# Kernel optimization log

Hardware: AMD Instinct MI355X
Metric: run time of the kernel (lower is better)

## Reference

```python
import jax, jax.numpy as jnp
import numpy as np
import math

B, N, EMB, DK = 4, 4096, 512, 64

def setup_inputs() -> dict:
    key = jax.random.key(0)
    ks = jax.random.split(key, 4)
    E = jax.random.normal(ks[0], (B, N, EMB), dtype=jnp.float32)
    mask = jnp.tril(jnp.ones((1, N, N), dtype=jnp.int32))  # causal mask, 0 = masked
    s = 1.0 / math.sqrt(EMB)
    wq_kernel = jax.random.normal(ks[1], (EMB, DK), dtype=jnp.float32) * s
    wk_kernel = jax.random.normal(ks[2], (EMB, DK), dtype=jnp.float32) * s
    wv_kernel = jax.random.normal(ks[3], (EMB, EMB), dtype=jnp.float32) * s
    return {
        "E": E, "mask": mask,
        "wq_kernel": wq_kernel, "wq_bias": jnp.zeros((DK,), jnp.float32),
        "wk_kernel": wk_kernel, "wk_bias": jnp.zeros((DK,), jnp.float32),
        "wv_kernel": wv_kernel, "wv_bias": jnp.zeros((EMB,), jnp.float32),
    }

def reference(E, mask, wq_kernel, wq_bias, wk_kernel, wk_bias, wv_kernel, wv_bias):
    # Dense projections (flax Dense: x @ kernel + bias)
    Q = jnp.einsum('bne,ed->bnd', E, wq_kernel) + wq_bias   # [B,N,DK]
    K = jnp.einsum('bne,ed->bnd', E, wk_kernel) + wk_bias   # [B,N,DK]
    V = jnp.einsum('bne,ed->bnd', E, wv_kernel) + wv_bias   # [B,N,EMB]
    scores = jnp.einsum('bqd,bkd->bqk', Q, K) / math.sqrt(Q.shape[-1])  # [B,N,N]
    scores = jnp.where(mask == 0, float('-inf'), scores)
    attention = jax.nn.softmax(scores, axis=-1)
    return jnp.einsum('bqk,bke->bqe', attention, V)  # [B,N,EMB]
```

## Files before the change

### kernel.cpp

```cpp
#include <hip/hip_runtime.h>
#include <hip/hip_bf16.h>

typedef float f32x4 __attribute__((ext_vector_type(4)));
typedef __bf16 bf16x8 __attribute__((ext_vector_type(8)));
typedef __bf16 bf16x4 __attribute__((ext_vector_type(4)));
typedef unsigned short ushort4v __attribute__((ext_vector_type(4)));
typedef unsigned short ushort8v __attribute__((ext_vector_type(8)));

#define MFMA16(a, b, c) __builtin_amdgcn_mfma_f32_16x16x32_bf16((a), (b), (c), 0, 0, 0)

__device__ __forceinline__ unsigned short f2bf(float f) {
    union { float f; unsigned int u; } v; v.f = f;
    unsigned int r = (v.u + 0x7fffu + ((v.u >> 16) & 1u)) >> 16;
    return (unsigned short)r;
}
__device__ __forceinline__ int imin(int a, int b) { return a < b ? a : b; }
__device__ __forceinline__ float fexp2(float x) {
    float r; asm("v_exp_f32 %0, %1" : "=v"(r) : "v"(x)); return r;
}

__device__ __forceinline__ void ldsbar() {
    asm volatile("s_waitcnt lgkmcnt(0)" ::: "memory");
    __builtin_amdgcn_s_barrier();
}

__global__ __launch_bounds__(256) void prep_w(const float* __restrict__ wq,
                                              const float* __restrict__ wk,
                                              const float* __restrict__ wv,
                                              unsigned short* __restrict__ Fqk,
                                              unsigned short* __restrict__ Fv)
{
    const int t = blockIdx.x * 256 + threadIdx.x;
    if (t < 8192) {
        const int lane = t & 63, kt = (t >> 6) & 15, ct = t >> 10;
        const int g = lane >> 4, li = lane & 15;
        const int c = ct * 16 + li;
        const int k0 = kt * 32 + g * 8;
        ushort8v u;
        if (c < 64) {
#pragma unroll
            for (int j = 0; j < 8; ++j) u[j] = f2bf(wq[(size_t)(k0 + j) * 64 + c]);
        } else {
#pragma unroll
            for (int j = 0; j < 8; ++j) u[j] = f2bf(wk[(size_t)(k0 + j) * 64 + (c - 64)]);
        }
        *(ushort8v*)&Fqk[(size_t)t * 8] = u;
    } else {
        const int t2 = t - 8192;
        const int lane = t2 & 63, kt = (t2 >> 6) & 15, ct = t2 >> 10;
        const int g = lane >> 4, li = lane & 15;
        const int c = ct * 16 + li;
        const int k0 = kt * 32 + g * 8;
        ushort8v u;
#pragma unroll
        for (int j = 0; j < 8; ++j) u[j] = f2bf(wv[(size_t)(k0 + j) * 512 + c]);
        *(ushort8v*)&Fv[(size_t)t2 * 8] = u;
    }
}

__global__ __launch_bounds__(512) void proj_kernel(const float* __restrict__ E,
        const unsigned short* __restrict__ Fqk, const unsigned short* __restrict__ Fv,
        const float* __restrict__ bq, const float* __restrict__ bk, const float* __restrict__ bv,
        unsigned short* __restrict__ Qb, unsigned short* __restrict__ Kb,
        unsigned short* __restrict__ Vt)
{
    __shared__ __align__(16) unsigned short Al[2][128][40];

    const int tid = threadIdx.x;
    const int w = tid >> 6, l = tid & 63, g = l >> 4, li = l & 15;
    const int wm = w >> 2, wn = w & 3;
    const int bx = blockIdx.x, by = blockIdx.y;
    const int row0 = bx * 128;
    const int arow = tid >> 2, ak = (tid & 3) * 8;
    const float* ebase = &E[(size_t)(row0 + arow) * 512 + ak];
    const float QSCALE = 0.125f * 1.4426950408889634f;

#define LOAD_E(kt, dst)                                                          \
    {                                                                            \
        const float* ep = ebase + (kt) * 32;                                     \
        f32x4 v0 = *(const f32x4*)ep;                                            \
        f32x4 v1 = *(const f32x4*)(ep + 4);                                      \
        _Pragma("unroll")                                                        \
        for (int j = 0; j < 4; ++j) { dst[j] = f2bf(v0[j]); dst[4 + j] = f2bf(v1[j]); } \
    }

    if (by == 0) {
        f32x4 acc[4][2];
#pragma unroll
        for (int mb = 0; mb < 4; ++mb)
#pragma unroll
            for (int nb = 0; nb < 2; ++nb) acc[mb][nb] = (f32x4)0.0f;

        bf16x8 bw[2], bwn[2];
        {
            ushort8v e0; LOAD_E(0, e0);
            *(ushort8v*)&Al[0][arow][ak] = e0;
#pragma unroll
            for (int nb = 0; nb < 2; ++nb) {
                const int ct = wn * 2 + nb;
                bw[nb] = *(const bf16x8*)&Fqk[((size_t)(ct * 16 + 0) * 64 + l) * 8];
            }
        }
        ldsbar();

        for (int kt = 0; kt < 16; ++kt) {
            const int buf = kt & 1;
            ushort8v en;
            if (kt < 15) LOAD_E(kt + 1, en);
            const int ktn = imin(kt + 1, 15);
#pragma unroll
            for (int nb = 0; nb < 2; ++nb) {
                const int ct = wn * 2 + nb;
                bwn[nb] = *(const bf16x8*)&Fqk[((size_t)(ct * 16 + ktn) * 64 + l) * 8];
            }
            bf16x8 af[4];
#pragma unroll
            for (int mb = 0; mb < 4; ++mb)
                af[mb] = *(const bf16x8*)&Al[buf][wm * 64 + mb * 16 + li][8 * g];
#pragma unroll
            for (int mb = 0; mb < 4; ++mb)
#pragma unroll
                for (int nb = 0; nb < 2; ++nb) acc[mb][nb] = MFMA16(af[mb], bw[nb], acc[mb][nb]);
            if (kt < 15) *(ushort8v*)&Al[buf ^ 1][arow][ak] = en;
            ldsbar();
            bw[0] = bwn[0]; bw[1] = bwn[1];
        }

#pragma unroll
        for (int mb = 0; mb < 4; ++mb) {
#pragma unroll
            for (int nb = 0; nb < 2; ++nb) {
                const int coll = wn * 32 + nb * 16 + li;
                const int grow0 = row0 + wm * 64 + mb * 16 + 4 * g;
                if (coll < 64) {
                    const float bb = bq[coll];
#pragma unroll
                    for (int r = 0; r < 4; ++r)
                        Qb[(size_t)(grow0 + r) * 64 + coll] = f2bf((acc[mb][nb][r] + bb) * QSCALE);
                } else {
                    const float bb = bk[coll - 64];
#pragma unroll
                    for (int r = 0; r < 4; ++r)
                        Kb[(size_t)(grow0 + r) * 64 + (coll - 64)] = f2bf(acc[mb][nb][r] + bb);
                }
            }
        }
    } else {
        const int vy = by - 1;
        f32x4 acc[4][4];
#pragma unroll
        for (int mb = 0; mb < 4; ++mb)
#pragma unroll
            for (int nb = 0; nb < 4; ++nb) acc[mb][nb] = (f32x4)0.0f;

        bf16x8 bw[4], bwn[4];
        {
            ushort8v e0; LOAD_E(0, e0);
            *(ushort8v*)&Al[0][arow][ak] = e0;
#pragma unroll
            for (int nb = 0; nb < 4; ++nb) {
                const int ct = vy * 16 + wn * 4 + nb;
                bw[nb] = *(const bf16x8*)&Fv[((size_t)(ct * 16 + 0) * 64 + l) * 8];
            }
        }
        ldsbar();

        for (int kt = 0; kt < 16; ++kt) {
            const int buf = kt & 1;
            ushort8v en;
            if (kt < 15) LOAD_E(kt + 1, en);
            const int ktn = imin(kt + 1, 15);
#pragma unroll
            for (int nb = 0; nb < 4; ++nb) {
                const int ct = vy * 16 + wn * 4 + nb;
                bwn[nb] = *(const bf16x8*)&Fv[((size_t)(ct * 16 + ktn) * 64 + l) * 8];
            }
            bf16x8 af[4];
#pragma unroll
            for (int mb = 0; mb < 4; ++mb)
                af[mb] = *(const bf16x8*)&Al[buf][wm * 64 + mb * 16 + li][8 * g];
#pragma unroll
            for (int mb = 0; mb < 4; ++mb)
#pragma unroll
                for (int nb = 0; nb < 4; ++nb) acc[mb][nb] = MFMA16(af[mb], bw[nb], acc[mb][nb]);
            if (kt < 15) *(ushort8v*)&Al[buf ^ 1][arow][ak] = en;
            ldsbar();
#pragma unroll
            for (int nb = 0; nb < 4; ++nb) bw[nb] = bwn[nb];
        }

#pragma unroll
        for (int mb = 0; mb < 4; ++mb) {
#pragma unroll
            for (int nb = 0; nb < 4; ++nb) {
                const int col = vy * 256 + wn * 64 + nb * 16 + li;
                const int grow0 = row0 + wm * 64 + mb * 16 + 4 * g;
                const float bb = bv[col];
                ushort4v u;
#pragma unroll
                for (int r = 0; r < 4; ++r) u[r] = f2bf(acc[mb][nb][r] + bb);
                const int bbatch = grow0 >> 12, n = grow0 & 4095;
                *(ushort4v*)(Vt + ((size_t)bbatch * 512 + col) * 4096 + n) = u;
            }
        }
    }
#undef LOAD_E
}

__global__ __launch_bounds__(256) void attn_kernel(const unsigned short* __restrict__ Qb,
                                                   const unsigned short* __restrict__ Kb,
                                                   const unsigned short* __restrict__ Vt,
                                                   float* __restrict__ out)
{
    __shared__ __align__(16) unsigned short Kl[2][64][64];
    __shared__ __align__(16) unsigned short Pl[2][64][76];
    __shared__ float scl[2][64];
    __shared__ __align__(16) float dfl[2][4];
    __shared__ float lsum_l[64];

    const int tid = threadIdx.x;
    const int w = tid >> 6, lane = tid & 63, g = lane >> 4, li = lane & 15;
    const int bid = blockIdx.x;
    const int x = bid >> 4, b = (bid >> 2) & 3, ch = bid & 3;
    const int k4 = x >> 4, r4 = x & 15;
    const int qt = (k4 == 0) ? r4 : (k4 == 1) ? (63 - r4) : (k4 == 2) ? (16 + r4) : (47 - r4);
    const int q0 = qt * 64;
    const int niter = qt + 1;
    const int qrow = 16 * w + li;

    const unsigned short* qptr = Qb + ((size_t)(b * 4096 + q0 + qrow)) * 64 + 8 * g;
    const bf16x8 QA0 = *(const bf16x8*)qptr;
    const bf16x8 QA1 = *(const bf16x8*)(qptr + 32);

    float m_r = -INFINITY, l_r = 0.0f;
    f32x4 Of[4][2];
#pragma unroll
    for (int qb = 0; qb < 4; ++qb) { Of[qb][0] = (f32x4)0.0f; Of[qb][1] = (f32x4)0.0f; }

    const int cglob = ch * 128 + w * 32 + li;
    const unsigned short* vbase = Vt + ((size_t)(b * 512 + cglob)) * 4096 + 8 * g;

    const int krow = tid >> 3, kch = tid & 7;
    const unsigned short* kgb = Kb + ((size_t)(b * 4096 + krow)) * 64 + kch * 8;
    const int kslot = (kch ^ (krow & 7)) * 8;

    {
        ushort8v v0 = *(const ushort8v*)(kgb);
        ushort8v v1 = *(const ushort8v*)(kgb + 32 * 64);
        *(ushort8v*)&Kl[0][krow][kslot] = v0;
        *(ushort8v*)&Kl[0][krow + 32][kslot] = v1;
    }
    ldsbar();

    for (int j = 0; j < niter; ++j) {
        const int buf = j & 1;
        const size_t kv0 = (size_t)j * 64;
        const bool havenext = (j + 1 < niter);

        const size_t kvn = (size_t)imin(j + 1, qt) * 4096;
        ushort8v kn0 = *(const ushort8v*)(kgb + kvn);
        ushort8v kn1 = *(const ushort8v*)(kgb + kvn + 32 * 64);

        bf16x8 VA[2][2];
#pragma unroll
        for (int cf = 0; cf < 2; ++cf)
#pragma unroll
            for (int ks = 0; ks < 2; ++ks)
                VA[cf][ks] = *(const bf16x8*)(vbase + (size_t)cf * 16 * 4096 + kv0 + ks * 32);

        f32x4 S[4];
        {
            const unsigned short(*Kt)[64] = Kl[buf];
            __builtin_amdgcn_s_setprio(1);
#pragma unroll
            for (int cb = 0; cb < 4; ++cb) {
                const int row = cb * 16 + li;
                bf16x8 K0 = *(const bf16x8*)&Kt[row][((g) ^ (row & 7)) * 8];
                bf16x8 K1 = *(const bf16x8*)&Kt[row][((4 + g) ^ (row & 7)) * 8];
                f32x4 s = (f32x4)0.0f;
                s = MFMA16(K0, QA0, s);
                s = MFMA16(K1, QA1, s);
                S[cb] = s;
            }
            __builtin_amdgcn_s_setprio(0);
        }
        if (j == qt) {
#pragma unroll
            for (int cb = 0; cb < 4; ++cb)
#pragma unroll
                for (int rr = 0; rr < 4; ++rr)
                    if (cb * 16 + 4 * g + rr > qrow) S[cb][rr] = -1e30f;
        }
        f32x4 m4 = S[0];
#pragma unroll
        for (int cb = 1; cb < 4; ++cb)
#pragma unroll
            for (int rr = 0; rr < 4; ++rr) m4[rr] = fmaxf(m4[rr], S[cb][rr]);
        float pm = fmaxf(fmaxf(m4[0], m4[1]), fmaxf(m4[2], m4[3]));
        pm = fmaxf(pm, __shfl_xor(pm, 16));
        pm = fmaxf(pm, __shfl_xor(pm, 32));

        const bool nore = __all(pm - m_r <= 8.0f);
        float sc = 1.0f;
        if (!nore) {
            const float mn = fmaxf(m_r, pm);
            sc = fexp2(m_r - mn);
            m_r = mn;
        }
        float rs = 0.0f;
#pragma unroll
        for (int cb = 0; cb < 4; ++cb) {
            bf16x4 pk;
#pragma unroll
            for (int rr = 0; rr < 4; ++rr) {
                const float pv = fexp2(S[cb][rr] - m_r);
                rs += pv;
                pk[rr] = (__bf16)pv;
            }
            *(bf16x4*)&Pl[buf][qrow][cb * 16 + 4 * g] = pk;
        }
        rs += __shfl_xor(rs, 16);
        rs += __shfl_xor(rs, 32);
        l_r = l_r * sc + rs;
        if (g == 0) scl[buf][qrow] = sc;
        if (lane == 0) dfl[buf][w] = nore ? 1.0f : 0.0f;

        if (havenext) {
            *(ushort8v*)&Kl[buf ^ 1][krow][kslot] = kn0;
            *(ushort8v*)&Kl[buf ^ 1][krow + 32][kslot] = kn1;
        }
        ldsbar();

        f32x4 df = *(const f32x4*)&dfl[buf][0];
        const bool allskip = (df[0] + df[1] + df[2] + df[3]) == 4.0f;
        __builtin_amdgcn_s_setprio(1);
#pragma unroll
        for (int qb = 0; qb < 4; ++qb) {
            bf16x8 PA0 = *(const bf16x8*)&Pl[buf][qb * 16 + li][8 * g];
            bf16x8 PA1 = *(const bf16x8*)&Pl[buf][qb * 16 + li][32 + 8 * g];
            if (!allskip) {
                f32x4 scv = *(const f32x4*)&scl[buf][qb * 16 + 4 * g];
#pragma unroll
                for (int cf = 0; cf < 2; ++cf)
#pragma unroll
                    for (int rr = 0; rr < 4; ++rr) Of[qb][cf][rr] *= scv[rr];
            }
#pragma unroll
            for (int cf = 0; cf < 2; ++cf) {
                f32x4 o = Of[qb][cf];
                o = MFMA16(PA0, VA[cf][0], o);
                o = MFMA16(PA1, VA[cf][1], o);
                Of[qb][cf] = o;
            }
        }
        __builtin_amdgcn_s_setprio(0);
    }

    if (g == 0) lsum_l[qrow] = l_r;
    ldsbar();

    float* obase = out + (size_t)(b * 4096 + q0 + 4 * g) * 512 + cglob;
#pragma unroll
    for (int qb = 0; qb < 4; ++qb) {
        f32x4 lv = *(const f32x4*)&lsum_l[qb * 16 + 4 * g];
#pragma unroll
        for (int cf = 0; cf < 2; ++cf)
#pragma unroll
            for (int rr = 0; rr < 4; ++rr)
                obase[(size_t)(qb * 16 + rr) * 512 + cf * 16] = Of[qb][cf][rr] / lv[rr];
    }
}

extern "C" void kernel_launch(void* const* d_in, const int* in_sizes, int n_in,
                              void* d_out, int out_size, void* d_ws, size_t ws_size,
                              hipStream_t stream)
{
    (void)in_sizes; (void)n_in; (void)out_size; (void)ws_size;
    const float* E  = (const float*)d_in[0];
    const float* wq = (const float*)d_in[2];
    const float* bq = (const float*)d_in[3];
    const float* wk = (const float*)d_in[4];
    const float* bk = (const float*)d_in[5];
    const float* wv = (const float*)d_in[6];
    const float* bv = (const float*)d_in[7];

    const size_t qk_elems = (size_t)4 * 4096 * 64;
    const size_t vt_elems = (size_t)4 * 512 * 4096;

    unsigned short* Qb  = (unsigned short*)d_ws;
    unsigned short* Kb  = Qb + qk_elems;
    unsigned short* Vt  = Kb + qk_elems;
    unsigned short* Fqk = Vt + vt_elems;
    unsigned short* Fv  = Fqk + (size_t)8192 * 8;
    float* out = (float*)d_out;

    prep_w<<<dim3(160), 256, 0, stream>>>(wq, wk, wv, Fqk, Fv);
    proj_kernel<<<dim3(128, 3), 512, 0, stream>>>(E, Fqk, Fv, bq, bk, bv, Qb, Kb, Vt);
    attn_kernel<<<dim3(1024), 256, 0, stream>>>(Qb, Kb, Vt, out);
}
```

Baseline: 119.3 us.

## Process 128-key tiles per iteration in causal attention with a single LDS buffer

Each attention loop iteration now covers 128 keys instead of 64, which halves the trip count and the per-iteration softmax and bookkeeping overhead. The double-buffered K and P arrays in LDS are replaced by single buffers, with two barriers per iteration. V fragments are now loaded after the softmax barrier rather than at the top of the iteration. The trade-offs are more exposed V load latency, loss of K/P double-buffer overlap, and wasted masked work on the last tile when the query-tile index is even.

```diff
diff --git a/kernel.cpp b/kernel.cpp
--- a/kernel.cpp
+++ b/kernel.cpp
@@ -212,10 +212,10 @@
                                                    const unsigned short* __restrict__ Vt,
                                                    float* __restrict__ out)
 {
-    __shared__ __align__(16) unsigned short Kl[2][64][64];
-    __shared__ __align__(16) unsigned short Pl[2][64][76];
-    __shared__ float scl[2][64];
-    __shared__ __align__(16) float dfl[2][4];
+    __shared__ __align__(16) unsigned short Kl[128][64];
+    __shared__ __align__(16) unsigned short Pl[64][140];
+    __shared__ float scl[64];
+    __shared__ __align__(16) float dfl[4];
     __shared__ float lsum_l[64];
 
     const int tid = threadIdx.x;
@@ -225,7 +225,7 @@
     const int k4 = x >> 4, r4 = x & 15;
     const int qt = (k4 == 0) ? r4 : (k4 == 1) ? (63 - r4) : (k4 == 2) ? (16 + r4) : (47 - r4);
     const int q0 = qt * 64;
-    const int niter = qt + 1;
+    const int niter = (qt + 2) >> 1;
     const int qrow = 16 * w + li;
 
     const unsigned short* qptr = Qb + ((size_t)(b * 4096 + q0 + qrow)) * 64 + 8 * g;
@@ -245,38 +245,32 @@
     const int kslot = (kch ^ (krow & 7)) * 8;
 
     {
-        ushort8v v0 = *(const ushort8v*)(kgb);
-        ushort8v v1 = *(const ushort8v*)(kgb + 32 * 64);
-        *(ushort8v*)&Kl[0][krow][kslot] = v0;
-        *(ushort8v*)&Kl[0][krow + 32][kslot] = v1;
+#pragma unroll
+        for (int i = 0; i < 4; ++i) {
+            ushort8v v = *(const ushort8v*)(kgb + (size_t)(32 * i) * 64);
+            *(ushort8v*)&Kl[krow + 32 * i][kslot] = v;
+        }
     }
     ldsbar();
 
     for (int j = 0; j < niter; ++j) {
-        const int buf = j & 1;
-        const size_t kv0 = (size_t)j * 64;
+        const size_t kv0 = (size_t)j * 128;
         const bool havenext = (j + 1 < niter);
-
-        const size_t kvn = (size_t)imin(j + 1, qt) * 4096;
-        ushort8v kn0 = *(const ushort8v*)(kgb + kvn);
-        ushort8v kn1 = *(const ushort8v*)(kgb + kvn + 32 * 64);
-
-        bf16x8 VA[2][2];
-#pragma unroll
-        for (int cf = 0; cf < 2; ++cf)
-#pragma unroll
-            for (int ks = 0; ks < 2; ++ks)
-                VA[cf][ks] = *(const bf16x8*)(vbase + (size_t)cf * 16 * 4096 + kv0 + ks * 32);
-
-        f32x4 S[4];
+        const int jn = imin(j + 1, niter - 1);
+
+        ushort8v kn[4];
+#pragma unroll
+        for (int i = 0; i < 4; ++i)
+            kn[i] = *(const ushort8v*)(kgb + (size_t)(128 * jn + 32 * i) * 64);
+
+        f32x4 S[8];
         {
-            const unsigned short(*Kt)[64] = Kl[buf];
             __builtin_amdgcn_s_setprio(1);
 #pragma unroll
-            for (int cb = 0; cb < 4; ++cb) {
+            for (int cb = 0; cb < 8; ++cb) {
                 const int row = cb * 16 + li;
-                bf16x8 K0 = *(const bf16x8*)&Kt[row][((g) ^ (row & 7)) * 8];
-                bf16x8 K1 = *(const bf16x8*)&Kt[row][((4 + g) ^ (row & 7)) * 8];
+                bf16x8 K0 = *(const bf16x8*)&Kl[row][((g) ^ (row & 7)) * 8];
+                bf16x8 K1 = *(const bf16x8*)&Kl[row][((4 + g) ^ (row & 7)) * 8];
                 f32x4 s = (f32x4)0.0f;
                 s = MFMA16(K0, QA0, s);
                 s = MFMA16(K1, QA1, s);
@@ -284,16 +278,16 @@
             }
             __builtin_amdgcn_s_setprio(0);
         }
-        if (j == qt) {
-#pragma unroll
-            for (int cb = 0; cb < 4; ++cb)
+        if (j == niter - 1) {
+#pragma unroll
+            for (int cb = 0; cb < 8; ++cb)
 #pragma unroll
                 for (int rr = 0; rr < 4; ++rr)
-                    if (cb * 16 + 4 * g + rr > qrow) S[cb][rr] = -1e30f;
+                    if ((int)kv0 + cb * 16 + 4 * g + rr > q0 + qrow) S[cb][rr] = -1e30f;
         }
         f32x4 m4 = S[0];
 #pragma unroll
-        for (int cb = 1; cb < 4; ++cb)
+        for (int cb = 1; cb < 8; ++cb)
 #pragma unroll
             for (int rr = 0; rr < 4; ++rr) m4[rr] = fmaxf(m4[rr], S[cb][rr]);
         float pm = fmaxf(fmaxf(m4[0], m4[1]), fmaxf(m4[2], m4[3]));
@@ -309,7 +303,7 @@
         }
         float rs = 0.0f;
 #pragma unroll
-        for (int cb = 0; cb < 4; ++cb) {
+        for (int cb = 0; cb < 8; ++cb) {
             bf16x4 pk;
 #pragma unroll
             for (int rr = 0; rr < 4; ++rr) {
@@ -317,43 +311,53 @@
                 rs += pv;
                 pk[rr] = (__bf16)pv;
             }
-            *(bf16x4*)&Pl[buf][qrow][cb * 16 + 4 * g] = pk;
+            *(bf16x4*)&Pl[qrow][cb * 16 + 4 * g] = pk;
         }
         rs += __shfl_xor(rs, 16);
         rs += __shfl_xor(rs, 32);
         l_r = l_r * sc + rs;
-        if (g == 0) scl[buf][qrow] = sc;
-        if (lane == 0) dfl[buf][w] = nore ? 1.0f : 0.0f;
+        if (g == 0) scl[qrow] = sc;
+        if (lane == 0) dfl[w] = nore ? 1.0f : 0.0f;
+        ldsbar();
+
+        bf16x8 VA[4][2];
+#pragma unroll
+        for (int ks = 0; ks < 4; ++ks)
+#pragma unroll
+            for (int cf = 0; cf < 2; ++cf)
+                VA[ks][cf] = *(const bf16x8*)(vbase + (size_t)cf * 16 * 4096 + kv0 + ks * 32);
+
+        f32x4 df = *(const f32x4*)&dfl[0];
+        const bool allskip = (df[0] + df[1] + df[2] + df[3]) == 4.0f;
+        if (!allskip) {
+#pragma unroll
+            for (int qb = 0; qb < 4; ++qb) {
+                f32x4 scv = *(const f32x4*)&scl[qb * 16 + 4 * g];
+#pragma unroll
+                for (int cf = 0; cf < 2; ++cf)
+#pragma unroll
+                    for (int rr = 0; rr < 4; ++rr) Of[qb][cf][rr] *= scv[rr];
+            }
+        }
+        __builtin_amdgcn_s_setprio(1);
+#pragma unroll
+        for (int ks = 0; ks < 4; ++ks) {
+#pragma unroll
+            for (int qb = 0; qb < 4; ++qb) {
+                bf16x8 PA = *(const bf16x8*)&Pl[qb * 16 + li][32 * ks + 8 * g];
+#pragma unroll
+                for (int cf = 0; cf < 2; ++cf)
+                    Of[qb][cf] = MFMA16(PA, VA[ks][cf], Of[qb][cf]);
+            }
+        }
+        __builtin_amdgcn_s_setprio(0);
 
         if (havenext) {
-            *(ushort8v*)&Kl[buf ^ 1][krow][kslot] = kn0;
-            *(ushort8v*)&Kl[buf ^ 1][krow + 32][kslot] = kn1;
+#pragma unroll
+            for (int i = 0; i < 4; ++i)
+                *(ushort8v*)&Kl[krow + 32 * i][kslot] = kn[i];
         }
         ldsbar();
-
-        f32x4 df = *(const f32x4*)&dfl[buf][0];
-        const bool allskip = (df[0] + df[1] + df[2] + df[3]) == 4.0f;
-        __builtin_amdgcn_s_setprio(1);
-#pragma unroll
-        for (int qb = 0; qb < 4; ++qb) {
-            bf16x8 PA0 = *(const bf16x8*)&Pl[buf][qb * 16 + li][8 * g];
-            bf16x8 PA1 = *(const bf16x8*)&Pl[buf][qb * 16 + li][32 + 8 * g];
-            if (!allskip) {
-                f32x4 scv = *(const f32x4*)&scl[buf][qb * 16 + 4 * g];
-#pragma unroll
-                for (int cf = 0; cf < 2; ++cf)
-#pragma unroll
-                    for (int rr = 0; rr < 4; ++rr) Of[qb][cf][rr] *= scv[rr];
-            }
-#pragma unroll
-            for (int cf = 0; cf < 2; ++cf) {
-                f32x4 o = Of[qb][cf];
-                o = MFMA16(PA0, VA[cf][0], o);
-                o = MFMA16(PA1, VA[cf][1], o);
-                Of[qb][cf] = o;
-            }
-        }
-        __builtin_amdgcn_s_setprio(0);
     }
 
     if (g == 0) lsum_l[qrow] = l_r;
```

Result: slower. 140.1 us (+17.4%).
